# Optimization experiments

Hardware: AMD Instinct MI355X
Metric: run time of the kernel (lower is better)

Reference implementation:

```python
import jax, jax.numpy as jnp
import numpy as np

B, L, DIM, S, K = 2, 2048, 1024, 16, 3
INNER = DIM  # expand = 1 (module only runs with expand=1, see notes)


def setup_inputs() -> dict:
    key = jax.random.key(0)
    ks = jax.random.split(key, 10)
    f = lambda k, shape, s=0.02: jax.random.normal(k, shape, jnp.float32) * s
    return {
        "x": jax.random.normal(ks[0], (B, L, DIM), jnp.float32),
        "gamma": jnp.ones((DIM,), jnp.float32),
        "beta": jnp.zeros((DIM,), jnp.float32),
        "W_in": f(ks[1], (2 * INNER, DIM)),
        "conv_w": f(ks[2], (INNER, 1, K), 0.2),   # depthwise conv, OIL layout
        "W_x": f(ks[3], (2 * S, INNER)),
        "W_dt": f(ks[4], (INNER, DIM)),
        "b_dt": f(ks[5], (INNER,), 0.1),
        "A_log": jax.random.normal(ks[6], (INNER, S), jnp.float32),
        "D_param": jnp.ones((INNER,), jnp.float32),
        "W_out": f(ks[7], (DIM, INNER)),
    }


def reference(x, gamma, beta, W_in, conv_w, W_x, W_dt, b_dt, A_log, D_param, W_out):
    residual = x
    # LayerNorm
    mu = jnp.mean(x, axis=-1, keepdims=True)
    var = jnp.var(x, axis=-1, keepdims=True)
    h = (x - mu) / jnp.sqrt(var + 1e-5) * gamma + beta
    # in_proj + chunk
    xz = jnp.einsum('bld,ed->ble', h, W_in)
    inner = W_in.shape[0] // 2
    xx, z = xz[..., :inner], xz[..., inner:]
    # depthwise conv1d, padding (K-1)//2, no bias
    k = conv_w.shape[-1]
    pad = (k - 1) // 2
    xc = jax.lax.conv_general_dilated(
        xx.transpose(0, 2, 1), conv_w, window_strides=(1,),
        padding=[(pad, pad)], dimension_numbers=('NCL', 'OIL', 'NCL'),
        feature_group_count=inner).transpose(0, 2, 1)
    xc = jax.nn.silu(xc)
    # projections for dt, B, C
    dt = jnp.einsum('bld,ed->ble', xc, W_dt) + b_dt
    BC = jnp.einsum('bld,ed->ble', xc, W_x)
    s = A_log.shape[-1]
    Bm, Cm = BC[..., :s], BC[..., s:]
    # selective scan
    A = -jnp.exp(A_log)                               # (d, s)
    dt = jax.nn.softplus(dt)                          # (b, l, d)
    dA = jnp.exp(jnp.einsum('bld,ds->blds', dt, A))   # (b, l, d, s)
    dB = jnp.einsum('bld,bls->blds', dt, Bm)          # (b, l, d, s)

    def step(state, inputs):
        dA_t, dB_t, C_t = inputs                      # (b,d,s), (b,d,s), (b,s)
        state = state * dA_t + dB_t
        y_t = jnp.einsum('bds,bs->bd', state, C_t)
        return state, y_t

    init = jnp.zeros((x.shape[0], inner, s), xc.dtype)
    _, ys = jax.lax.scan(
        step, init,
        (dA.transpose(1, 0, 2, 3), dB.transpose(1, 0, 2, 3), Cm.transpose(1, 0, 2)))
    y = ys.transpose(1, 0, 2)                         # (b, l, d)
    # skip, gate, out projection, residual
    y = y + D_param * xc
    y = y * jax.nn.silu(z)
    out = jnp.einsum('bld,ed->ble', y, W_out)
    return out + residual
```

## Files before the change

kernel.cpp:

```cpp
#include <hip/hip_runtime.h>
#include <math.h>

#define BB 2
#define LL 2048
#define DIMV 1024
#define SSV 16
#define INNERV 1024
#define E2V 2048
#define MMV (BB*LL)
#define NCHUNK 64
#define CLEN 32

typedef __attribute__((ext_vector_type(8))) short short8;
typedef __attribute__((ext_vector_type(4))) float f32x4;

static __device__ __forceinline__ float4 ld4(const float* p){
  return *reinterpret_cast<const float4*>(p);
}
static __device__ __forceinline__ ushort f2bf(float x){
  unsigned u = __float_as_uint(x);
  unsigned r = (u + 0x7fffu + ((u >> 16) & 1u)) >> 16;
  return (ushort)r;
}
static __device__ __forceinline__ float bf2f(ushort h){
  return __uint_as_float(((unsigned)h) << 16);
}
static __device__ __forceinline__ void gld16(const void* g, void* l){
  __builtin_amdgcn_global_load_lds(
      (const __attribute__((address_space(1))) void*)g,
      (__attribute__((address_space(3))) void*)l, 16, 0, 0);
}

__global__ __launch_bounds__(256) void ln_init(
        const float* __restrict__ x, const float* __restrict__ gamma,
        const float* __restrict__ beta, ushort* __restrict__ hh,
        const float* __restrict__ W_in, const float* __restrict__ W_dt,
        const float* __restrict__ W_out, const float* __restrict__ wx,
        ushort* __restrict__ Wih, ushort* __restrict__ Wdh,
        ushort* __restrict__ Woh, float* __restrict__ wxt){
  __shared__ float red[8];
  if (blockIdx.x < 4224){
    int idx = blockIdx.x*256 + threadIdx.x;
    if (idx < 1024*1024){
      const float* src; ushort* dst; int i;
      if (idx < 512*1024){ src = W_in;  dst = Wih; i = idx; }
      else if (idx < 768*1024){ src = W_dt;  dst = Wdh; i = idx - 512*1024; }
      else { src = W_out; dst = Woh; i = idx - 768*1024; }
      float4 v = ld4(src + (size_t)i*4);
      ushort4 H;
      H.x=f2bf(v.x); H.y=f2bf(v.y); H.z=f2bf(v.z); H.w=f2bf(v.w);
      *reinterpret_cast<ushort4*>(dst + (size_t)i*4) = H;
    } else {
      int j = idx - 1024*1024;
      int e = j >> 10, k = j & 1023;
      wxt[k*32 + e] = wx[j];
    }
    return;
  }
  int row = blockIdx.x - 4224;
  int tid = threadIdx.x;
  const float* xr = x + (size_t)row*DIMV;
  float4 v = ld4(xr + tid*4);
  float s  = v.x+v.y+v.z+v.w;
  float s2 = v.x*v.x+v.y*v.y+v.z*v.z+v.w*v.w;
  for (int o=32;o;o>>=1){ s += __shfl_down(s,o); s2 += __shfl_down(s2,o); }
  int wid = tid>>6, lane = tid&63;
  if (lane==0){ red[wid]=s; red[4+wid]=s2; }
  __syncthreads();
  s  = red[0]+red[1]+red[2]+red[3];
  s2 = red[4]+red[5]+red[6]+red[7];
  float mu  = s*(1.f/DIMV);
  float var = s2*(1.f/DIMV) - mu*mu;
  float rstd = rsqrtf(var + 1e-5f);
  float4 g = ld4(gamma + tid*4), be = ld4(beta + tid*4);
  ushort4 H;
  H.x = f2bf((v.x-mu)*rstd*g.x + be.x);
  H.y = f2bf((v.y-mu)*rstd*g.y + be.y);
  H.z = f2bf((v.z-mu)*rstd*g.z + be.z);
  H.w = f2bf((v.w-mu)*rstd*g.w + be.w);
  *reinterpret_cast<ushort4*>(hh + (size_t)row*DIMV + tid*4) = H;
}

#define GBK 64
#define NKT 16

template<int EPI, int BN>
static __device__ __forceinline__ void gemm_body(ushort* lds,
    const ushort* __restrict__ A, const ushort* __restrict__ Bw,
    void* __restrict__ Co_, int N, const float* __restrict__ aux,
    int bm, int bn){
  const int t  = threadIdx.x;
  const int rr  = t >> 3;
  const int k16 = (t & 7) ^ (rr & 7);
  const ushort* gA = A  + (size_t)(bm + rr)*1024 + k16*8;
  const ushort* gB = Bw + (size_t)(bn + rr)*1024 + k16*8;
  const int wofs = (t >> 6) * 1024;

  const int l  = t & 63, wv = t >> 6;
  const int wm = wv & 1, wn = wv >> 1;
  const int fr = l & 15, kb = l >> 4;
  const int WN = BN/2;
  const int NF = BN/64;

  f32x4 acc[4][2*NF];
  #pragma unroll
  for (int m=0;m<4;m++){
    #pragma unroll
    for (int n=0;n<2*NF;n++) acc[m][n] = (f32x4){0.f,0.f,0.f,0.f};
  }

  char* Lb = (char*)lds;
  for (int kt = 0; kt < NKT; ++kt){
    const int ko = kt*GBK;
    gld16(gA + ko,           Lb +     0 + wofs);
    gld16(gA + ko + 32*1024, Lb +  4096 + wofs);
    gld16(gA + ko + 64*1024, Lb +  8192 + wofs);
    gld16(gA + ko + 96*1024, Lb + 12288 + wofs);
    gld16(gB + ko,           Lb + 16384 + wofs);
    gld16(gB + ko + 32*1024, Lb + 20480 + wofs);
    if (BN == 128){
      gld16(gB + ko + 64*1024, Lb + 24576 + wofs);
      gld16(gB + ko + 96*1024, Lb + 28672 + wofs);
    }
    __syncthreads();
    short8 a[4][2], b[2*NF][2];
    #pragma unroll
    for (int m=0;m<4;m++){
      int row = wm*64 + m*16 + fr;
      #pragma unroll
      for (int ks=0;ks<2;ks++)
        a[m][ks] = *(const short8*)(Lb + row*128 + (((ks*4+kb)^(fr&7))*16));
    }
    #pragma unroll
    for (int n=0;n<2*NF;n++){
      int row = wn*WN + n*16 + fr;
      #pragma unroll
      for (int ks=0;ks<2;ks++)
        b[n][ks] = *(const short8*)(Lb + 16384 + row*128 + (((ks*4+kb)^(fr&7))*16));
    }
    #pragma unroll
    for (int ks=0;ks<2;ks++){
      #pragma unroll
      for (int m=0;m<4;m++){
        #pragma unroll
        for (int n=0;n<2*NF;n++)
          acc[m][n] = __builtin_amdgcn_mfma_f32_16x16x32_bf16(a[m][ks], b[n][ks], acc[m][n], 0,0,0);
      }
    }
    __syncthreads();
  }

  #pragma unroll
  for (int m=0;m<4;m++){
    int row0 = bm + wm*64 + m*16 + kb*4;
    #pragma unroll
    for (int n=0;n<2*NF;n++){
      int col = bn + wn*WN + n*16 + fr;
      #pragma unroll
      for (int j=0;j<4;j++){
        int r = row0 + j;
        float v = acc[m][n][j];
        if (EPI==0){
          ((ushort*)Co_)[(size_t)r*N + col] = f2bf(v);
        } else if (EPI==1){
          v += aux[col];
          v = (v > 20.f) ? v : log1pf(__expf(v));
          ((ushort*)Co_)[(size_t)r*N + col] = f2bf(v);
        } else {
          v += aux[(size_t)r*N + col];
          ((float*)Co_)[(size_t)r*N + col] = v;
        }
      }
    }
  }
}

template<int EPI, int BN>
__global__ __launch_bounds__(256) void gemm_bf16(
    const ushort* __restrict__ A, const ushort* __restrict__ Bw,
    void* __restrict__ Co_, int N, const float* __restrict__ aux){
  __shared__ __align__(16) ushort lds[(128+BN)*GBK];
  gemm_body<EPI,BN>(lds, A, Bw, Co_, N, aux, blockIdx.y*128, blockIdx.x*BN);
}

static __device__ __forceinline__ void bc_body(ushort* sh, float* sw,
    const ushort* __restrict__ xch, const float* __restrict__ wxt,
    float* __restrict__ bc, int blk){
  int tid = threadIdx.x;
  int row0 = blk * 8;
  const ushort4* srcH = (const ushort4*)(xch + (size_t)row0*DIMV);
  #pragma unroll
  for (int i=0;i<8;i++)
    ((ushort4*)sh)[tid + i*256] = srcH[tid + i*256];
  int r = tid >> 5, e = tid & 31;
  float a0=0.f, a1=0.f, a2=0.f, a3=0.f;
  for (int kt=0; kt<8; ++kt){
    __syncthreads();
    const float4* wsrc = (const float4*)(wxt + kt*128*32);
    #pragma unroll
    for (int i=0;i<4;i++)
      ((float4*)sw)[tid + i*256] = wsrc[tid + i*256];
    __syncthreads();
    const ushort* xr = &sh[r*1024 + kt*128];
    #pragma unroll
    for (int k=0;k<128;k+=4){
      ushort4 xv = *(const ushort4*)&xr[k];
      a0 = fmaf(bf2f(xv.x), sw[(k+0)*32+e], a0);
      a1 = fmaf(bf2f(xv.y), sw[(k+1)*32+e], a1);
      a2 = fmaf(bf2f(xv.z), sw[(k+2)*32+e], a2);
      a3 = fmaf(bf2f(xv.w), sw[(k+3)*32+e], a3);
    }
  }
  bc[(size_t)(row0 + r)*32 + e] = (a0+a1)+(a2+a3);
}

__global__ __launch_bounds__(256) void fused_mid(
    const ushort* __restrict__ hh, const ushort* __restrict__ Wz,
    ushort* __restrict__ zh,
    const ushort* __restrict__ xch, const ushort* __restrict__ Wdh,
    ushort* __restrict__ dtb, const float* __restrict__ b_dt,
    const float* __restrict__ wxt, float* __restrict__ bcb){
  __shared__ __align__(16) ushort lds[16384];
  int bid = blockIdx.x;
  if (bid < 256){
    gemm_body<0,128>(lds, hh, Wz, zh, DIMV, nullptr, (bid>>3)*128, (bid&7)*128);
  } else if (bid < 768){
    int t2 = bid - 256;
    gemm_body<1,64>(lds, xch, Wdh, dtb, INNERV, b_dt, (t2>>4)*128, (t2&15)*64);
  } else {
    bc_body(lds, (float*)(lds + 8192), xch, wxt, bcb, bid - 768);
  }
}

__global__ __launch_bounds__(256) void conv_silu_kernel(const ushort* __restrict__ xxh,
        const float* __restrict__ cw, ushort* __restrict__ xch){
  int idx = blockIdx.x*256 + threadIdx.x;
  int d4  = idx & 255;
  int row = idx >> 8;
  int t = row & (LL-1);
  const ushort* p = xxh + (size_t)row*DIMV + d4*4;
  ushort4 u1 = *reinterpret_cast<const ushort4*>(p);
  ushort4 u0 = (t>0)    ? *reinterpret_cast<const ushort4*>(p - DIMV) : make_ushort4(0,0,0,0);
  ushort4 u2 = (t<LL-1) ? *reinterpret_cast<const ushort4*>(p + DIMV) : make_ushort4(0,0,0,0);
  int d = d4*4;
  float w[12];
  #pragma unroll
  for (int i=0;i<12;i++) w[i] = cw[d*3 + i];
  float4 o;
  o.x = bf2f(u0.x)*w[0] + bf2f(u1.x)*w[1]  + bf2f(u2.x)*w[2];
  o.y = bf2f(u0.y)*w[3] + bf2f(u1.y)*w[4]  + bf2f(u2.y)*w[5];
  o.z = bf2f(u0.z)*w[6] + bf2f(u1.z)*w[7]  + bf2f(u2.z)*w[8];
  o.w = bf2f(u0.w)*w[9] + bf2f(u1.w)*w[10] + bf2f(u2.w)*w[11];
  o.x = o.x / (1.f + __expf(-o.x));
  o.y = o.y / (1.f + __expf(-o.y));
  o.z = o.z / (1.f + __expf(-o.z));
  o.w = o.w / (1.f + __expf(-o.w));
  ushort4 H;
  H.x=f2bf(o.x); H.y=f2bf(o.y); H.z=f2bf(o.z); H.w=f2bf(o.w);
  *reinterpret_cast<ushort4*>(xch + (size_t)row*DIMV + d4*4) = H;
}

__global__ __launch_bounds__(256) void scan_p1(const ushort* __restrict__ dt,
        const float* __restrict__ bc, const float* __restrict__ A_log,
        ushort* __restrict__ F, ushort* __restrict__ P){
  __shared__ float sB[CLEN*32];
  int bid = blockIdx.x;
  int dblk = bid & 3;
  int c  = (bid >> 2) & (NCHUNK-1);
  int b  = bid >> 8;
  int tid = threadIdx.x;
  int d = dblk*256 + tid;
  int row0 = b*LL + c*CLEN;
  ((float4*)sB)[tid] = *((const float4*)(bc + (size_t)row0*32) + tid);
  float a[16];
  {
    const float4* ap = (const float4*)(A_log + d*16);
    #pragma unroll
    for (int q=0;q<4;q++){
      float4 v = ap[q];
      a[q*4+0]=-__expf(v.x); a[q*4+1]=-__expf(v.y);
      a[q*4+2]=-__expf(v.z); a[q*4+3]=-__expf(v.w);
    }
  }
  __syncthreads();
  float st[16];
  #pragma unroll
  for (int s=0;s<16;s++) st[s]=0.f;
  float sdt = 0.f;
  const ushort* dtp = dt + (size_t)row0*DIMV + d;
  for (int t=0;t<CLEN;t++){
    float dtv = bf2f(dtp[(size_t)t*DIMV]);
    sdt += dtv;
    float4 B0 = *(const float4*)&sB[t*32+0];
    float4 B1 = *(const float4*)&sB[t*32+4];
    float4 B2 = *(const float4*)&sB[t*32+8];
    float4 B3 = *(const float4*)&sB[t*32+12];
    float Bv[16] = {B0.x,B0.y,B0.z,B0.w,B1.x,B1.y,B1.z,B1.w,
                    B2.x,B2.y,B2.z,B2.w,B3.x,B3.y,B3.z,B3.w};
    #pragma unroll
    for (int s=0;s<16;s++){
      float dA = __expf(dtv*a[s]);
      st[s] = fmaf(st[s], dA, dtv*Bv[s]);
    }
  }
  size_t o = ((size_t)((b*NCHUNK + c)*DIMV + d))*16;
  #pragma unroll
  for (int q=0;q<4;q++){
    ushort4 fv, pv;
    fv.x=f2bf(st[q*4]);   fv.y=f2bf(st[q*4+1]);
    fv.z=f2bf(st[q*4+2]); fv.w=f2bf(st[q*4+3]);
    pv.x=f2bf(__expf(sdt*a[q*4]));   pv.y=f2bf(__expf(sdt*a[q*4+1]));
    pv.z=f2bf(__expf(sdt*a[q*4+2])); pv.w=f2bf(__expf(sdt*a[q*4+3]));
    *(ushort4*)(F + o + q*4) = fv;
    *(ushort4*)(P + o + q*4) = pv;
  }
}

__global__ __launch_bounds__(256) void scan_p2(const ushort* __restrict__ F,
        const ushort* __restrict__ P, ushort* __restrict__ E){
  int idx = blockIdx.x*256 + threadIdx.x;
  int b  = idx >> 14;
  int ds = idx & 16383;
  float e = 0.f;
  for (int c=0;c<NCHUNK;c++){
    size_t o = ((size_t)(b*NCHUNK + c) << 14) + ds;
    E[o] = f2bf(e);
    e = fmaf(bf2f(P[o]), e, bf2f(F[o]));
  }
}

__global__ __launch_bounds__(256) void scan_p3(const ushort* __restrict__ dt,
        const float* __restrict__ bc, const float* __restrict__ A_log,
        const ushort* __restrict__ E, const ushort* __restrict__ xch,
        const ushort* __restrict__ zh, const float* __restrict__ Dp,
        ushort* __restrict__ yh){
  __shared__ float sBC[CLEN*32];
  int bid = blockIdx.x;
  int dblk = bid & 3;
  int c  = (bid >> 2) & (NCHUNK-1);
  int b  = bid >> 8;
  int tid = threadIdx.x;
  int d = dblk*256 + tid;
  int row0 = b*LL + c*CLEN;
  ((float4*)sBC)[tid] = *((const float4*)(bc + (size_t)row0*32) + tid);
  float a[16];
  {
    const float4* ap = (const float4*)(A_log + d*16);
    #pragma unroll
    for (int q=0;q<4;q++){
      float4 v = ap[q];
      a[q*4+0]=-__expf(v.x); a[q*4+1]=-__expf(v.y);
      a[q*4+2]=-__expf(v.z); a[q*4+3]=-__expf(v.w);
    }
  }
  float st[16];
  {
    size_t o = ((size_t)((b*NCHUNK + c)*DIMV + d))*16;
    #pragma unroll
    for (int q=0;q<4;q++){
      ushort4 v = *(const ushort4*)(E + o + q*4);
      st[q*4]=bf2f(v.x); st[q*4+1]=bf2f(v.y); st[q*4+2]=bf2f(v.z); st[q*4+3]=bf2f(v.w);
    }
  }
  float Dv = Dp[d];
  __syncthreads();
  const ushort* dtp = dt + (size_t)row0*DIMV + d;
  for (int t=0;t<CLEN;t++){
    float dtv = bf2f(dtp[(size_t)t*DIMV]);
    float4 B0 = *(const float4*)&sBC[t*32+0];
    float4 B1 = *(const float4*)&sBC[t*32+4];
    float4 B2 = *(const float4*)&sBC[t*32+8];
    float4 B3 = *(const float4*)&sBC[t*32+12];
    float4 C0 = *(const float4*)&sBC[t*32+16];
    float4 C1 = *(const float4*)&sBC[t*32+20];
    float4 C2 = *(const float4*)&sBC[t*32+24];
    float4 C3 = *(const float4*)&sBC[t*32+28];
    float Bv[16] = {B0.x,B0.y,B0.z,B0.w,B1.x,B1.y,B1.z,B1.w,
                    B2.x,B2.y,B2.z,B2.w,B3.x,B3.y,B3.z,B3.w};
    float Cv[16] = {C0.x,C0.y,C0.z,C0.w,C1.x,C1.y,C1.z,C1.w,
                    C2.x,C2.y,C2.z,C2.w,C3.x,C3.y,C3.z,C3.w};
    float y = 0.f;
    #pragma unroll
    for (int s=0;s<16;s++){
      float dA = __expf(dtv*a[s]);
      st[s] = fmaf(st[s], dA, dtv*Bv[s]);
      y = fmaf(st[s], Cv[s], y);
    }
    int row = row0 + t;
    size_t ofs = (size_t)row*DIMV + d;
    float xcv = bf2f(xch[ofs]);
    float zv  = bf2f(zh[ofs]);
    float sz  = zv / (1.f + __expf(-zv));
    yh[ofs] = f2bf((y + Dv*xcv)*sz);
  }
}

extern "C" void kernel_launch(void* const* d_in, const int* in_sizes, int n_in,
                              void* d_out, int out_size, void* d_ws, size_t ws_size,
                              hipStream_t stream){
  const float* x     = (const float*)d_in[0];
  const float* gamma = (const float*)d_in[1];
  const float* beta  = (const float*)d_in[2];
  const float* W_in  = (const float*)d_in[3];
  const float* cw    = (const float*)d_in[4];
  const float* W_x   = (const float*)d_in[5];
  const float* W_dt  = (const float*)d_in[6];
  const float* b_dt  = (const float*)d_in[7];
  const float* A_log = (const float*)d_in[8];
  const float* Dp    = (const float*)d_in[9];
  const float* W_out = (const float*)d_in[10];
  float* out = (float*)d_out;
  float* ws  = (float*)d_ws;
  const size_t MB = (size_t)1 << 20;
  ushort* xxh = (ushort*)ws;
  ushort* zh  = (ushort*)(ws + 2*MB);
  ushort* hh  = (ushort*)(ws + 4*MB);
  ushort* yh  = (ushort*)(ws + 4*MB);
  ushort* xch = (ushort*)(ws + 6*MB);
  ushort* dtb = (ushort*)(ws + 8*MB);
  ushort* F   = (ushort*)(ws + 10*MB);
  ushort* P   = (ushort*)(ws + 11*MB);
  ushort* E   = (ushort*)(ws + 12*MB);
  ushort* Wih = (ushort*)(ws + 13*MB);
  ushort* Wdh = (ushort*)(ws + 14*MB);
  ushort* Woh = (ushort*)(ws + 14*MB + 512*1024);
  float*  bcb = ws + 15*MB;
  float*  wxt = ws + 15*MB + 128*1024;

  ln_init<<<4224 + MMV, 256, 0, stream>>>(x, gamma, beta, hh,
                                          W_in, W_dt, W_out, W_x,
                                          Wih, Wdh, Woh, wxt);
  gemm_bf16<0,128><<<dim3(8, MMV/128), 256, 0, stream>>>(hh, Wih, xxh, DIMV, nullptr);
  conv_silu_kernel<<<(MMV*(DIMV/4))/256, 256, 0, stream>>>(xxh, cw, xch);
  fused_mid<<<1280, 256, 0, stream>>>(hh, Wih + (size_t)1024*1024, zh,
                                      xch, Wdh, dtb, b_dt, wxt, bcb);
  scan_p1<<<BB*NCHUNK*(DIMV/256), 256, 0, stream>>>(dtb, bcb, A_log, F, P);
  scan_p2<<<(BB*DIMV*SSV)/256, 256, 0, stream>>>(F, P, E);
  scan_p3<<<BB*NCHUNK*(DIMV/256), 256, 0, stream>>>(dtb, bcb, A_log, E, xch, zh, Dp, yh);
  gemm_bf16<2,64><<<dim3(DIMV/64, MMV/128), 256, 0, stream>>>(yh, Woh, out, DIMV, x);
}
```

Measured before the change: 181.6 us.

## Compute full in_proj (x and z) in one GEMM and split dt/BC kernel

The in_proj GEMM now produces both x and z halves in one launch with N=2048 into an interleaved xz buffer, instead of computing z later inside the fused mid kernel. The mid kernel then only holds the dt GEMM and the B/C projection, with the BC path's weight tile halved to 64 rows so shared memory fits a smaller 12288-element buffer. Conv and scan_p3 read from the wider-strided xz buffer. This gives a larger, more regular first GEMM and a lighter, more occupant mid kernel, at the cost of strided z reads in scan_p3 and twice as many sync steps in bc_body.

```diff
diff --git a/kernel.cpp b/kernel.cpp
--- a/kernel.cpp
+++ b/kernel.cpp
@@ -194,16 +194,15 @@
     ((ushort4*)sh)[tid + i*256] = srcH[tid + i*256];
   int r = tid >> 5, e = tid & 31;
   float a0=0.f, a1=0.f, a2=0.f, a3=0.f;
-  for (int kt=0; kt<8; ++kt){
+  for (int kt=0; kt<16; ++kt){
     __syncthreads();
-    const float4* wsrc = (const float4*)(wxt + kt*128*32);
-    #pragma unroll
-    for (int i=0;i<4;i++)
-      ((float4*)sw)[tid + i*256] = wsrc[tid + i*256];
+    const float4* wsrc = (const float4*)(wxt + kt*64*32);
+    ((float4*)sw)[tid]       = wsrc[tid];
+    ((float4*)sw)[tid + 256] = wsrc[tid + 256];
     __syncthreads();
-    const ushort* xr = &sh[r*1024 + kt*128];
-    #pragma unroll
-    for (int k=0;k<128;k+=4){
+    const ushort* xr = &sh[r*1024 + kt*64];
+    #pragma unroll
+    for (int k=0;k<64;k+=4){
       ushort4 xv = *(const ushort4*)&xr[k];
       a0 = fmaf(bf2f(xv.x), sw[(k+0)*32+e], a0);
       a1 = fmaf(bf2f(xv.y), sw[(k+1)*32+e], a1);
@@ -214,34 +213,28 @@
   bc[(size_t)(row0 + r)*32 + e] = (a0+a1)+(a2+a3);
 }
 
-__global__ __launch_bounds__(256) void fused_mid(
-    const ushort* __restrict__ hh, const ushort* __restrict__ Wz,
-    ushort* __restrict__ zh,
+__global__ __launch_bounds__(256) void gemm1_bc(
     const ushort* __restrict__ xch, const ushort* __restrict__ Wdh,
     ushort* __restrict__ dtb, const float* __restrict__ b_dt,
     const float* __restrict__ wxt, float* __restrict__ bcb){
-  __shared__ __align__(16) ushort lds[16384];
-  int bid = blockIdx.x;
-  if (bid < 256){
-    gemm_body<0,128>(lds, hh, Wz, zh, DIMV, nullptr, (bid>>3)*128, (bid&7)*128);
-  } else if (bid < 768){
-    int t2 = bid - 256;
-    gemm_body<1,64>(lds, xch, Wdh, dtb, INNERV, b_dt, (t2>>4)*128, (t2&15)*64);
+  __shared__ __align__(16) ushort lds[12288];
+  if (blockIdx.y < 32){
+    gemm_body<1,64>(lds, xch, Wdh, dtb, INNERV, b_dt, blockIdx.y*128, blockIdx.x*64);
   } else {
-    bc_body(lds, (float*)(lds + 8192), xch, wxt, bcb, bid - 768);
-  }
-}
-
-__global__ __launch_bounds__(256) void conv_silu_kernel(const ushort* __restrict__ xxh,
+    bc_body(lds, (float*)(lds + 8192), xch, wxt, bcb, (blockIdx.y-32)*16 + blockIdx.x);
+  }
+}
+
+__global__ __launch_bounds__(256) void conv_silu_kernel(const ushort* __restrict__ xz,
         const float* __restrict__ cw, ushort* __restrict__ xch){
   int idx = blockIdx.x*256 + threadIdx.x;
   int d4  = idx & 255;
   int row = idx >> 8;
   int t = row & (LL-1);
-  const ushort* p = xxh + (size_t)row*DIMV + d4*4;
+  const ushort* p = xz + (size_t)row*E2V + d4*4;
   ushort4 u1 = *reinterpret_cast<const ushort4*>(p);
-  ushort4 u0 = (t>0)    ? *reinterpret_cast<const ushort4*>(p - DIMV) : make_ushort4(0,0,0,0);
-  ushort4 u2 = (t<LL-1) ? *reinterpret_cast<const ushort4*>(p + DIMV) : make_ushort4(0,0,0,0);
+  ushort4 u0 = (t>0)    ? *reinterpret_cast<const ushort4*>(p - E2V) : make_ushort4(0,0,0,0);
+  ushort4 u2 = (t<LL-1) ? *reinterpret_cast<const ushort4*>(p + E2V) : make_ushort4(0,0,0,0);
   int d = d4*4;
   float w[12];
   #pragma unroll
@@ -332,7 +325,7 @@
 __global__ __launch_bounds__(256) void scan_p3(const ushort* __restrict__ dt,
         const float* __restrict__ bc, const float* __restrict__ A_log,
         const ushort* __restrict__ E, const ushort* __restrict__ xch,
-        const ushort* __restrict__ zh, const float* __restrict__ Dp,
+        const ushort* __restrict__ xz, const float* __restrict__ Dp,
         ushort* __restrict__ yh){
   __shared__ float sBC[CLEN*32];
   int bid = blockIdx.x;
@@ -389,7 +382,7 @@
     int row = row0 + t;
     size_t ofs = (size_t)row*DIMV + d;
     float xcv = bf2f(xch[ofs]);
-    float zv  = bf2f(zh[ofs]);
+    float zv  = bf2f(xz[(size_t)row*E2V + INNERV + d]);
     float sz  = zv / (1.f + __expf(-zv));
     yh[ofs] = f2bf((y + Dv*xcv)*sz);
   }
@@ -412,8 +405,7 @@
   float* out = (float*)d_out;
   float* ws  = (float*)d_ws;
   const size_t MB = (size_t)1 << 20;
-  ushort* xxh = (ushort*)ws;
-  ushort* zh  = (ushort*)(ws + 2*MB);
+  ushort* xzh = (ushort*)ws;
   ushort* hh  = (ushort*)(ws + 4*MB);
   ushort* yh  = (ushort*)(ws + 4*MB);
   ushort* xch = (ushort*)(ws + 6*MB);
@@ -430,12 +422,11 @@
   ln_init<<<4224 + MMV, 256, 0, stream>>>(x, gamma, beta, hh,
                                           W_in, W_dt, W_out, W_x,
                                           Wih, Wdh, Woh, wxt);
-  gemm_bf16<0,128><<<dim3(8, MMV/128), 256, 0, stream>>>(hh, Wih, xxh, DIMV, nullptr);
-  conv_silu_kernel<<<(MMV*(DIMV/4))/256, 256, 0, stream>>>(xxh, cw, xch);
-  fused_mid<<<1280, 256, 0, stream>>>(hh, Wih + (size_t)1024*1024, zh,
-                                      xch, Wdh, dtb, b_dt, wxt, bcb);
+  gemm_bf16<0,128><<<dim3(E2V/128, MMV/128), 256, 0, stream>>>(hh, Wih, xzh, E2V, nullptr);
+  conv_silu_kernel<<<(MMV*(DIMV/4))/256, 256, 0, stream>>>(xzh, cw, xch);
+  gemm1_bc<<<dim3(16, 64), 256, 0, stream>>>(xch, Wdh, dtb, b_dt, wxt, bcb);
   scan_p1<<<BB*NCHUNK*(DIMV/256), 256, 0, stream>>>(dtb, bcb, A_log, F, P);
   scan_p2<<<(BB*DIMV*SSV)/256, 256, 0, stream>>>(F, P, E);
-  scan_p3<<<BB*NCHUNK*(DIMV/256), 256, 0, stream>>>(dtb, bcb, A_log, E, xch, zh, Dp, yh);
+  scan_p3<<<BB*NCHUNK*(DIMV/256), 256, 0, stream>>>(dtb, bcb, A_log, E, xch, xzh, Dp, yh);
   gemm_bf16<2,64><<<dim3(DIMV/64, MMV/128), 256, 0, stream>>>(yh, Woh, out, DIMV, x);
 }
```

After: 154.4 us. -15.0%, faster.
